# Kernel tuning notes

Measured on AMD Instinct MI355X. Metric: run time of the kernel, lower is better.

Reference implementation:

```python
import jax, jax.numpy as jnp
import numpy as np

K = 32   # tokens_per_obs (hard-coded in module)
V = 512  # vocab_size

def setup_inputs() -> dict:
    key = jax.random.key(0)
    ks = jax.random.split(key, 10)
    s = 0.02  # small init scale for numerical sanity
    return {
        "x": jax.random.normal(ks[0], (4096, 512), jnp.float32),
        "enc_w1": jax.random.normal(ks[1], (512, 512), jnp.float32) * s,
        "enc_b1": jnp.zeros((512,), jnp.float32),
        "enc_w2": jax.random.normal(ks[2], (512, 16384), jnp.float32) * s,
        "enc_b2": jnp.zeros((16384,), jnp.float32),
        "codebook": jax.random.uniform(ks[3], (16384, 256), jnp.float32, -1.0 / V, 1.0 / V),
        "dec_w1": jax.random.normal(ks[4], (256, 512), jnp.float32) * s,
        "dec_b1": jnp.zeros((512,), jnp.float32),
        "dec_w2": jax.random.normal(ks[5], (512, 512), jnp.float32) * s,
        "dec_b2": jnp.zeros((512,), jnp.float32),
    }

def reference(x, enc_w1, enc_b1, enc_w2, enc_b2, codebook,
              dec_w1, dec_b1, dec_w2, dec_b2):
    b = x.shape[0]
    # encoder MLP -> logits z of shape (b, K*V)
    h = jax.nn.relu(x @ enc_w1 + enc_b1)
    z = h @ enc_w2 + enc_b2
    zl = z.reshape(b, K, V)                      # (b, K, V) per-block logits
    # categorical sample per token block
    tokens = jax.random.categorical(jax.random.key(1), zl, axis=-1)  # (b, K) int
    p = jax.nn.softmax(zl, axis=-1).reshape(b, K * V)
    oh = jax.nn.one_hot(tokens, V, dtype=p.dtype).reshape(b, K * V)
    # straight-through: forward value == one-hot, gradient flows through p
    st = p + jax.lax.stop_gradient(oh - p)
    z_q = st @ codebook                          # (b, embed_dim) = sum of K code rows
    # decoder MLP -> reconstruction
    rec = jax.nn.relu(z_q @ dec_w1 + dec_b1) @ dec_w2 + dec_b2
    return z, z_q, rec
```

## Files before the change

### kernel.cpp

```cpp
#include <hip/hip_runtime.h>
#include <hip/hip_bf16.h>
#include <math.h>
#include <stdint.h>


#define BATCH 4096
#define KTOK  32
#define VOCAB 512
#define DMODEL 512
#define ZDIM  16384
#define EDIM  256
#define MARGIN 0.03125f

typedef __attribute__((ext_vector_type(8))) short short8v;
typedef __attribute__((ext_vector_type(4))) float f32x4;

__device__ __forceinline__ void threefry2x32(uint32_t k0, uint32_t k1,
                                             uint32_t x0, uint32_t x1,
                                             uint32_t& y0, uint32_t& y1) {
    uint32_t ks0 = k0, ks1 = k1, ks2 = k0 ^ k1 ^ 0x1BD11BDAu;
    x0 += ks0; x1 += ks1;
#define TFR(r) { x0 += x1; x1 = __builtin_rotateleft32(x1, r); x1 ^= x0; }
    TFR(13) TFR(15) TFR(26) TFR(6)
    x0 += ks1; x1 += ks2 + 1u;
    TFR(17) TFR(29) TFR(16) TFR(24)
    x0 += ks2; x1 += ks0 + 2u;
    TFR(13) TFR(15) TFR(26) TFR(6)
    x0 += ks0; x1 += ks1 + 3u;
    TFR(17) TFR(29) TFR(16) TFR(24)
    x0 += ks1; x1 += ks2 + 4u;
    TFR(13) TFR(15) TFR(26) TFR(6)
    x0 += ks2; x1 += ks0 + 5u;
#undef TFR
    y0 = x0; y1 = x1;
}

__device__ __forceinline__ void threefry4x(uint32_t e,
                                           uint32_t& o0, uint32_t& o1,
                                           uint32_t& o2, uint32_t& o3) {
    const uint32_t KS2 = 0x1BD11BDBu;
    uint32_t xa = 0u, ya = e + 1u;
    uint32_t xb = 0u, yb = e + 2u;
    uint32_t xc = 0u, yc = e + 3u;
    uint32_t xd = 0u, yd = e + 4u;
#define RR(r) \
    xa += ya; xb += yb; xc += yc; xd += yd; \
    ya = __builtin_rotateleft32(ya, r) ^ xa; \
    yb = __builtin_rotateleft32(yb, r) ^ xb; \
    yc = __builtin_rotateleft32(yc, r) ^ xc; \
    yd = __builtin_rotateleft32(yd, r) ^ xd;
    RR(13) RR(15) RR(26) RR(6)
    xa += 1u; xb += 1u; xc += 1u; xd += 1u;
    ya += KS2 + 1u; yb += KS2 + 1u; yc += KS2 + 1u; yd += KS2 + 1u;
    RR(17) RR(29) RR(16) RR(24)
    xa += KS2; xb += KS2; xc += KS2; xd += KS2;
    ya += 2u; yb += 2u; yc += 2u; yd += 2u;
    RR(13) RR(15) RR(26) RR(6)
    ya += 4u; yb += 4u; yc += 4u; yd += 4u;
    RR(17) RR(29) RR(16) RR(24)
    xa += 1u; xb += 1u; xc += 1u; xd += 1u;
    ya += KS2 + 4u; yb += KS2 + 4u; yc += KS2 + 4u; yd += KS2 + 4u;
    RR(13) RR(15) RR(26) RR(6)
    xa += KS2; xb += KS2; xc += KS2; xd += KS2;
    ya += 5u; yb += 5u; yc += 5u; yd += 5u;
#undef RR
    o0 = xa ^ ya; o1 = xb ^ yb; o2 = xc ^ yc; o3 = xd ^ yd;
}

__device__ __forceinline__ float jax_gumbel(uint64_t e) {
    const float TINY = 1.17549435e-38f;
    uint32_t y0, y1;
    threefry2x32(0u, 1u, (uint32_t)(e >> 32), (uint32_t)(e & 0xffffffffull), y0, y1);
    uint32_t bits = y0 ^ y1;
    float u = __uint_as_float(0x3f800000u | (bits >> 9)) - 1.0f;
    u = u * 1.0f + TINY;
    u = fmaxf(TINY, u);
    return -logf(-logf(u));
}

__device__ __forceinline__ float gumbel_from_bits(uint32_t bits) {
    const float TINY = 1.17549435e-38f;
    const float LN2 = 0.69314718056f;
    float f = __uint_as_float(0x3f800000u | (bits >> 9));
    float u = f - 1.0f;
    float d = 2.0f - f;
    u = fmaxf(u, TINY);
    float e_hw = -LN2 * __builtin_amdgcn_logf(u);
    float e_poly = d * fmaf(d, fmaf(d, 0.33333333f, 0.5f), 1.0f);
    float e = (d < 0.002f) ? e_poly : e_hw;
    return -LN2 * __builtin_amdgcn_logf(e);
}

__device__ __forceinline__ float fast_gumbel(uint32_t e32) {
    uint32_t y0, y1;
    threefry2x32(0u, 1u, 0u, e32, y0, y1);
    return gumbel_from_bits(y0 ^ y1);
}

__device__ __forceinline__ unsigned short f32_to_bf16_rne(float f) {
    uint32_t u = __float_as_uint(f);
    uint32_t r = (u + 0x7fffu + ((u >> 16) & 1u)) >> 16;
    return (unsigned short)r;
}

__device__ __forceinline__ void top2_push(float& s1, float& s2, int& v1,
                                          float s, int v) {
    if (s > s1 || (s == s1 && v < v1)) { s2 = s1; s1 = s; v1 = v; }
    else s2 = fmaxf(s2, s);
}
__device__ __forceinline__ void top2_merge(float& s1, float& s2, int& v1,
                                           float os1, float os2, int ov1) {
    if (os1 > s1 || (os1 == s1 && ov1 < v1)) {
        s2 = fmaxf(s1, os2);
        s1 = os1; v1 = ov1;
    } else {
        s2 = fmaxf(s2, os1);
    }
}

__device__ __forceinline__ void gload16(const unsigned short* src,
                                        unsigned short* lds_base) {
    __builtin_amdgcn_global_load_lds(
        (const __attribute__((address_space(1))) unsigned int*)src,
        (__attribute__((address_space(3))) unsigned int*)lds_base, 16, 0, 0);
}

template<bool RELU>
__global__ __launch_bounds__(256)
void gemm_f32_64(const float* __restrict__ A, const float* __restrict__ B,
                 const float* __restrict__ bias, float* __restrict__ C,
                 unsigned short* __restrict__ Cb,
                 int M, int N, int K) {
    constexpr int BK = 16;
    __shared__ __align__(16) float As[BK][68];
    __shared__ __align__(16) float Bs[BK][68];

    const int tid = threadIdx.x;
    const int tx = tid % 16;
    const int ty = tid / 16;
    const int brow = blockIdx.y * 64;
    const int bcol = blockIdx.x * 64;

    float acc[4][4] = {};

    for (int k0 = 0; k0 < K; k0 += BK) {
        {
            int r = tid >> 2, c4 = tid & 3;
            float4 v = *(const float4*)&A[(size_t)(brow + r) * K + k0 + c4 * 4];
            As[c4 * 4 + 0][r] = v.x;
            As[c4 * 4 + 1][r] = v.y;
            As[c4 * 4 + 2][r] = v.z;
            As[c4 * 4 + 3][r] = v.w;
        }
        {
            int r = tid >> 4, c4 = tid & 15;
            *(float4*)&Bs[r][c4 * 4] = *(const float4*)&B[(size_t)(k0 + r) * N + bcol + c4 * 4];
        }
        __syncthreads();

#pragma unroll
        for (int kk = 0; kk < BK; ++kk) {
            float a[4], b[4];
            *(float4*)&a[0] = *(const float4*)&As[kk][ty * 4];
            *(float4*)&b[0] = *(const float4*)&Bs[kk][tx * 4];
#pragma unroll
            for (int i = 0; i < 4; ++i)
#pragma unroll
                for (int j = 0; j < 4; ++j)
                    acc[i][j] = fmaf(a[i], b[j], acc[i][j]);
        }
        __syncthreads();
    }

#pragma unroll
    for (int i = 0; i < 4; ++i) {
        int row = brow + ty * 4 + i;
        int col = bcol + tx * 4;
        float4 v;
        v.x = acc[i][0] + bias[col + 0];
        v.y = acc[i][1] + bias[col + 1];
        v.z = acc[i][2] + bias[col + 2];
        v.w = acc[i][3] + bias[col + 3];
        if (RELU) {
            v.x = fmaxf(v.x, 0.0f); v.y = fmaxf(v.y, 0.0f);
            v.z = fmaxf(v.z, 0.0f); v.w = fmaxf(v.w, 0.0f);
        }
        *(float4*)&C[(size_t)row * N + col] = v;
        if (Cb) {
            ushort4 o;
            o.x = f32_to_bf16_rne(v.x);
            o.y = f32_to_bf16_rne(v.y);
            o.z = f32_to_bf16_rne(v.z);
            o.w = f32_to_bf16_rne(v.w);
            *(ushort4*)&Cb[(size_t)row * N + col] = o;
        }
    }
}

template<bool RELU>
__global__ __launch_bounds__(256)
void gemm_f32(const float* __restrict__ A, const float* __restrict__ B,
              const float* __restrict__ bias, float* __restrict__ C,
              int M, int N, int K) {
    constexpr int BM = 128, BN = 128, BK = 16, TM = 8, TN = 8;
    __shared__ __align__(16) float As[BK][BM + 4];
    __shared__ __align__(16) float Bs[BK][BN + 4];

    const int tid = threadIdx.x;
    const int tx = tid % (BN / TN);
    const int ty = tid / (BN / TN);
    const int brow = blockIdx.y * BM;
    const int bcol = blockIdx.x * BN;

    float acc[TM][TN] = {};

    for (int k0 = 0; k0 < K; k0 += BK) {
#pragma unroll
        for (int f = tid; f < BM * BK / 4; f += 256) {
            int r = f / (BK / 4);
            int c4 = f % (BK / 4);
            float4 v = *(const float4*)&A[(size_t)(brow + r) * K + k0 + c4 * 4];
            As[c4 * 4 + 0][r] = v.x;
            As[c4 * 4 + 1][r] = v.y;
            As[c4 * 4 + 2][r] = v.z;
            As[c4 * 4 + 3][r] = v.w;
        }
#pragma unroll
        for (int f = tid; f < BK * BN / 4; f += 256) {
            int r = f / (BN / 4);
            int c4 = f % (BN / 4);
            *(float4*)&Bs[r][c4 * 4] = *(const float4*)&B[(size_t)(k0 + r) * N + bcol + c4 * 4];
        }
        __syncthreads();

#pragma unroll
        for (int kk = 0; kk < BK; ++kk) {
            float a[TM], b[TN];
            *(float4*)&a[0] = *(const float4*)&As[kk][ty * TM];
            *(float4*)&a[4] = *(const float4*)&As[kk][ty * TM + 4];
            *(float4*)&b[0] = *(const float4*)&Bs[kk][tx * TN];
            *(float4*)&b[4] = *(const float4*)&Bs[kk][tx * TN + 4];
#pragma unroll
            for (int i = 0; i < TM; ++i)
#pragma unroll
                for (int j = 0; j < TN; ++j)
                    acc[i][j] = fmaf(a[i], b[j], acc[i][j]);
        }
        __syncthreads();
    }

#pragma unroll
    for (int i = 0; i < TM; ++i) {
        int row = brow + ty * TM + i;
#pragma unroll
        for (int j = 0; j < TN; j += 4) {
            int col = bcol + tx * TN + j;
            float4 v;
            v.x = acc[i][j + 0] + bias[col + 0];
            v.y = acc[i][j + 1] + bias[col + 1];
            v.z = acc[i][j + 2] + bias[col + 2];
            v.w = acc[i][j + 3] + bias[col + 3];
            if (RELU) {
                v.x = fmaxf(v.x, 0.0f); v.y = fmaxf(v.y, 0.0f);
                v.z = fmaxf(v.z, 0.0f); v.w = fmaxf(v.w, 0.0f);
            }
            *(float4*)&C[(size_t)row * N + col] = v;
        }
    }
}

__global__ __launch_bounds__(256)
void transpose_w2(const float* __restrict__ src, unsigned short* __restrict__ dstb,
                  float* __restrict__ dstf, int R, int C, int writeF) {
    __shared__ float tile[32][33];
    const int c0 = blockIdx.x * 32, r0 = blockIdx.y * 32;
    const int tx = threadIdx.x % 32, ty = threadIdx.x / 32;
#pragma unroll
    for (int i = ty; i < 32; i += 8)
        tile[i][tx] = src[(size_t)(r0 + i) * C + c0 + tx];
    __syncthreads();
#pragma unroll
    for (int i = ty; i < 32; i += 8) {
        float v = tile[tx][i];
        size_t o = (size_t)(c0 + i) * R + r0 + tx;
        dstb[o] = f32_to_bf16_rne(v);
        if (writeF) dstf[o] = v;
    }
}

__global__ __launch_bounds__(256)
void gemm_mfma_bf16(const unsigned short* __restrict__ A,
                    const unsigned short* __restrict__ Bt,
                    const float* __restrict__ bias,
                    float* __restrict__ C,
                    int M, int N, int K) {
    constexpr int BM = 128, BN = 128, BK = 32;
    constexpr int TSZ = BM * BK;
    __shared__ unsigned short As[2 * TSZ];
    __shared__ unsigned short Bs[2 * TSZ];

    const int lid = blockIdx.y * gridDim.x + blockIdx.x;
    const int xcd = lid & 7;
    const int kk2 = lid >> 3;
    const int rpx = gridDim.y >> 3;
    const int by = xcd * rpx + (kk2 % rpx);
    const int bx = kk2 / rpx;

    const int tid = threadIdx.x;
    const int wid = tid >> 6;
    const int lane = tid & 63;
    const int wr = wid >> 1, wc = wid & 1;
    const int l15 = lane & 15, lq = lane >> 4;
    const int brow = by * BM;
    const int bcol = bx * BN;

    const int g1 = tid;
    const int g2 = tid + 256;
    const size_t a1 = (size_t)(brow + (g1 >> 2)) * K + (g1 & 3) * 8;
    const size_t a2 = (size_t)(brow + (g2 >> 2)) * K + (g2 & 3) * 8;
    const size_t b1 = (size_t)(bcol + (g1 >> 2)) * K + (g1 & 3) * 8;
    const size_t b2 = (size_t)(bcol + (g2 >> 2)) * K + (g2 & 3) * 8;
    const int asOff1 = wid * 64 * 8;
    const int asOff2 = (256 + wid * 64) * 8;

    f32x4 acc[4][4];
#pragma unroll
    for (int m = 0; m < 4; ++m)
#pragma unroll
        for (int n = 0; n < 4; ++n) acc[m][n] = (f32x4){0.f, 0.f, 0.f, 0.f};

    const int NK = K / BK;
    gload16(A + a1, As + asOff1);
    gload16(A + a2, As + asOff2);
    gload16(Bt + b1, Bs + asOff1);
    gload16(Bt + b2, Bs + asOff2);
    __syncthreads();

    int buf = 0;
    for (int kt = 0; kt < NK; ++kt) {
        if (kt + 1 < NK) {
            const int k0 = (kt + 1) * BK;
            const int o = (buf ^ 1) * TSZ;
            gload16(A + a1 + k0, As + o + asOff1);
            gload16(A + a2 + k0, As + o + asOff2);
            gload16(Bt + b1 + k0, Bs + o + asOff1);
            gload16(Bt + b2 + k0, Bs + o + asOff2);
        }
        const int cb = buf * TSZ;
        short8v af[4], bf[4];
#pragma unroll
        for (int m = 0; m < 4; ++m)
            af[m] = *(const short8v*)&As[cb + (wr * 64 + m * 16 + l15) * BK + lq * 8];
#pragma unroll
        for (int n = 0; n < 4; ++n)
            bf[n] = *(const short8v*)&Bs[cb + (wc * 64 + n * 16 + l15) * BK + lq * 8];
#pragma unroll
        for (int m = 0; m < 4; ++m)
#pragma unroll
            for (int n = 0; n < 4; ++n)
                acc[m][n] = __builtin_amdgcn_mfma_f32_16x16x32_bf16(
                    af[m], bf[n], acc[m][n], 0, 0, 0);
        __syncthreads();
        buf ^= 1;
    }

#pragma unroll
    for (int m = 0; m < 4; ++m) {
#pragma unroll
        for (int n = 0; n < 4; ++n) {
            int col = bcol + wc * 64 + n * 16 + l15;
            float bv = bias[col];
#pragma unroll
            for (int r = 0; r < 4; ++r) {
                int row = brow + wr * 64 + m * 16 + lq * 4 + r;
                C[(size_t)row * N + col] = acc[m][n][r] + bv;
            }
        }
    }
}

__global__ __launch_bounds__(256)
void sample_tokens_ilp(const float* __restrict__ z, int* __restrict__ tokens,
                       float* __restrict__ s1v, int* __restrict__ amb,
                       int* __restrict__ ambCount) {
    const int wave = threadIdx.x >> 6;
    const int lane = threadIdx.x & 63;
    const uint32_t t = blockIdx.x * 4 + wave;
    const float* zr = z + (size_t)t * VOCAB;

    float s1 = -INFINITY, s2 = -INFINITY;
    int v1 = VOCAB;
#pragma unroll
    for (int half = 0; half < 2; ++half) {
        const int e0 = half * 256 + lane * 4;
        const float4 zv = *(const float4*)&zr[e0];
        uint32_t b0, b1, b2, b3;
        threefry4x(t * (uint32_t)VOCAB + (uint32_t)e0, b0, b1, b2, b3);
        const float g0 = gumbel_from_bits(b0);
        const float g1 = gumbel_from_bits(b1);
        const float g2 = gumbel_from_bits(b2);
        const float g3 = gumbel_from_bits(b3);
        top2_push(s1, s2, v1, zv.x + g0, e0 + 0);
        top2_push(s1, s2, v1, zv.y + g1, e0 + 1);
        top2_push(s1, s2, v1, zv.z + g2, e0 + 2);
        top2_push(s1, s2, v1, zv.w + g3, e0 + 3);
    }
#pragma unroll
    for (int off = 32; off > 0; off >>= 1) {
        float os1 = __shfl_xor(s1, off);
        int ov1 = __shfl_xor(v1, off);
        float os2 = __shfl_xor(s2, off);
        top2_merge(s1, s2, v1, os1, os2, ov1);
    }
    if (lane == 0) {
        tokens[t] = v1;
        s1v[t] = s1;
        if (s1 - s2 < MARGIN) {
            int idx = atomicAdd(ambCount, 1);
            amb[idx] = (int)t;
        }
    }
}

__global__ __launch_bounds__(64)
void refine_tokens2(const float* __restrict__ z, const float* __restrict__ h,
                    const float* __restrict__ w2t, const float* __restrict__ eb2,
                    const int* __restrict__ amb, const int* __restrict__ ambCount,
                    const float* __restrict__ s1v, int* __restrict__ tok) {
    __shared__ float hrow[DMODEL];
    __shared__ int candv[64];
    const int cnt = *ambCount;
    const int lane = threadIdx.x;

    for (int i = blockIdx.x; i < cnt; i += gridDim.x) {
        const int t = amb[i];
        const int b = t >> 5;
        const int kb = t & 31;
        const float* zr = z + (size_t)t * VOCAB;
        const float s1 = s1v[t];

        {
            float4 hv0 = *(const float4*)&h[(size_t)b * DMODEL + lane * 8];
            float4 hv1 = *(const float4*)&h[(size_t)b * DMODEL + lane * 8 + 4];
            *(float4*)&hrow[lane * 8] = hv0;
            *(float4*)&hrow[lane * 8 + 4] = hv1;
        }

        int base = 0;
#pragma unroll
        for (int half = 0; half < 2; ++half) {
            int e0 = half * 256 + lane * 4;
            float4 zv = *(const float4*)&zr[e0];
            float zs[4] = {zv.x, zv.y, zv.z, zv.w};
#pragma unroll
            for (int j = 0; j < 4; ++j) {
                int v = e0 + j;
                float s = zs[j] + fast_gumbel((uint32_t)t * VOCAB + v);
                bool pred = (s >= s1 - MARGIN);
                unsigned long long mask = __ballot(pred);
                if (pred) {
                    int slot = base + __popcll(mask & ((1ull << lane) - 1ull));
                    if (slot < 64) candv[slot] = v;
                }
                base += __popcll(mask);
            }
        }
        __syncthreads();
        const int ncand = base < 64 ? base : 64;

        float bestE = -INFINITY;
        int bestV = VOCAB;
        if (lane < ncand) {
            const int v = candv[lane];
            const int n = kb * VOCAB + v;
            const float* wr_ = w2t + (size_t)n * DMODEL;
            float acc = 0.f;
#pragma unroll 8
            for (int k = 0; k < DMODEL; ++k)
                acc = fmaf(hrow[k], wr_[k], acc);
            bestE = acc + eb2[n] + jax_gumbel((uint64_t)t * VOCAB + v);
            bestV = v;
        }
#pragma unroll
        for (int off = 32; off > 0; off >>= 1) {
            float oe = __shfl_down(bestE, off);
            int ov = __shfl_down(bestV, off);
            if (oe > bestE || (oe == bestE && ov < bestV)) { bestE = oe; bestV = ov; }
        }
        if (lane == 0) tok[t] = bestV;
        __syncthreads();
    }
}

__global__ __launch_bounds__(256)
void sample_tokens_simple(const float* __restrict__ z, int* __restrict__ tokens) {
    const int wave = threadIdx.x >> 6;
    const int lane = threadIdx.x & 63;
    const size_t t = (size_t)blockIdx.x * 4 + wave;
    const float* zr = z + t * VOCAB;
    float zv[8];
    *(float4*)&zv[0] = *(const float4*)&zr[lane * 8];
    *(float4*)&zv[4] = *(const float4*)&zr[lane * 8 + 4];
    const uint64_t ebase = t * (uint64_t)VOCAB + (uint64_t)lane * 8;
    float best = -INFINITY;
    int bestv = 0;
#pragma unroll
    for (int j = 0; j < 8; ++j) {
        float g = jax_gumbel(ebase + j);
        float s = zv[j] + g;
        int v = lane * 8 + j;
        if (s > best || (s == best && v < bestv)) { best = s; bestv = v; }
    }
#pragma unroll
    for (int off = 32; off > 0; off >>= 1) {
        float ob = __shfl_down(best, off);
        int ov = __shfl_down(bestv, off);
        if (ob > best || (ob == best && ov < bestv)) { best = ob; bestv = ov; }
    }
    if (lane == 0) tokens[t] = bestv;
}

__global__ __launch_bounds__(64)
void zero_count(int* p) { if (threadIdx.x == 0) *p = 0; }

__global__ __launch_bounds__(256)
void gather_zq(const int* __restrict__ tokens, const float* __restrict__ codebook,
               float* __restrict__ zq) {
    const int b = blockIdx.x;
    const int d = threadIdx.x;
    float s = 0.0f;
#pragma unroll
    for (int k = 0; k < KTOK; ++k) {
        int tok = tokens[b * KTOK + k];
        s += codebook[(size_t)(k * VOCAB + tok) * EDIM + d];
    }
    zq[(size_t)b * EDIM + d] = s;
}

extern "C" void kernel_launch(void* const* d_in, const int* in_sizes, int n_in,
                              void* d_out, int out_size, void* d_ws, size_t ws_size,
                              hipStream_t stream) {
    const float* x   = (const float*)d_in[0];
    const float* ew1 = (const float*)d_in[1];
    const float* eb1 = (const float*)d_in[2];
    const float* ew2 = (const float*)d_in[3];
    const float* eb2 = (const float*)d_in[4];
    const float* cb  = (const float*)d_in[5];
    const float* dw1 = (const float*)d_in[6];
    const float* db1 = (const float*)d_in[7];
    const float* dw2 = (const float*)d_in[8];
    const float* db2 = (const float*)d_in[9];

    float* out = (float*)d_out;
    float* z   = out;
    float* zq  = out + (size_t)BATCH * ZDIM;
    float* rec = zq + (size_t)BATCH * EDIM;

    char* ws = (char*)d_ws;
    float* h    = (float*)(ws);
    float* h2   = (float*)(ws + 8388608);
    unsigned short* hb   = (unsigned short*)(ws + 16777216);
    unsigned short* w2bt = (unsigned short*)(ws + 20971520);
    float* w2t  = (float*)(ws + 37748736);
    char* tail = ws + 71303168;
    const size_t WS_NEED2 = 71303168 + 1572864 + 256;
    const bool fast2 = ws_size >= WS_NEED2;
    if (!fast2) tail = ws + 16777216;
    int*   tok  = (int*)(tail);
    float* s1v  = (float*)(tail + 524288);
    int*   amb  = (int*)(tail + 1048576);
    int*   cnt  = (int*)(tail + 1572864);

    dim3 blk(256);

    gemm_f32_64<true ><<<dim3(DMODEL / 64, BATCH / 64), blk, 0, stream>>>(
        x, ew1, eb1, h, fast2 ? hb : (unsigned short*)nullptr,
        BATCH, DMODEL, DMODEL);

    if (fast2) {
        transpose_w2<<<dim3(ZDIM / 32, DMODEL / 32), blk, 0, stream>>>(
            ew2, w2bt, w2t, DMODEL, ZDIM, 1);
        zero_count<<<dim3(1), dim3(64), 0, stream>>>(cnt);
        gemm_mfma_bf16<<<dim3(ZDIM / 128, BATCH / 128), blk, 0, stream>>>(
            hb, w2bt, eb2, z, BATCH, ZDIM, DMODEL);
        sample_tokens_ilp<<<dim3(BATCH * KTOK / 4), blk, 0, stream>>>(
            z, tok, s1v, amb, cnt);
        refine_tokens2<<<dim3(4096), dim3(64), 0, stream>>>(
            z, h, w2t, eb2, amb, cnt, s1v, tok);
    } else {
        gemm_f32<false><<<dim3(ZDIM / 128, BATCH / 128), blk, 0, stream>>>(
            h, ew2, eb2, z, BATCH, ZDIM, DMODEL);
        sample_tokens_simple<<<dim3(BATCH * KTOK / 4), blk, 0, stream>>>(z, tok);
    }

    gather_zq<<<dim3(BATCH), blk, 0, stream>>>(tok, cb, zq);

    gemm_f32_64<true ><<<dim3(DMODEL / 64, BATCH / 64), blk, 0, stream>>>(
        zq, dw1, db1, h2, nullptr, BATCH, DMODEL, EDIM);
    gemm_f32_64<false><<<dim3(DMODEL / 64, BATCH / 64), blk, 0, stream>>>(
        h2, dw2, db2, rec, nullptr, BATCH, DMODEL, DMODEL);
}
```

Baseline: 435.1 us.

## Triple-buffer MFMA GEMM, use bf16 MFMA for decoder, simplify sampling top-1

```diff
diff --git a/kernel.cpp b/kernel.cpp
--- a/kernel.cpp
+++ b/kernel.cpp
@@ -103,21 +103,6 @@
     return (unsigned short)r;
 }
 
-__device__ __forceinline__ void top2_push(float& s1, float& s2, int& v1,
-                                          float s, int v) {
-    if (s > s1 || (s == s1 && v < v1)) { s2 = s1; s1 = s; v1 = v; }
-    else s2 = fmaxf(s2, s);
-}
-__device__ __forceinline__ void top2_merge(float& s1, float& s2, int& v1,
-                                           float os1, float os2, int ov1) {
-    if (os1 > s1 || (os1 == s1 && ov1 < v1)) {
-        s2 = fmaxf(s1, os2);
-        s1 = os1; v1 = ov1;
-    } else {
-        s2 = fmaxf(s2, os1);
-    }
-}
-
 __device__ __forceinline__ void gload16(const unsigned short* src,
                                         unsigned short* lds_base) {
     __builtin_amdgcn_global_load_lds(
@@ -288,16 +273,17 @@
     }
 }
 
+template<bool RELU, bool WF32, bool WBF16>
 __global__ __launch_bounds__(256)
-void gemm_mfma_bf16(const unsigned short* __restrict__ A,
-                    const unsigned short* __restrict__ Bt,
-                    const float* __restrict__ bias,
-                    float* __restrict__ C,
-                    int M, int N, int K) {
+void gemm_mfma(const unsigned short* __restrict__ A,
+               const unsigned short* __restrict__ Bt,
+               const float* __restrict__ bias,
+               float* __restrict__ C, unsigned short* __restrict__ Cb,
+               int M, int N, int K) {
     constexpr int BM = 128, BN = 128, BK = 32;
     constexpr int TSZ = BM * BK;
-    __shared__ unsigned short As[2 * TSZ];
-    __shared__ unsigned short Bs[2 * TSZ];
+    __shared__ unsigned short As[3 * TSZ];
+    __shared__ unsigned short Bs[3 * TSZ];
 
     const int lid = blockIdx.y * gridDim.x + blockIdx.x;
     const int xcd = lid & 7;
@@ -320,8 +306,8 @@
     const size_t a2 = (size_t)(brow + (g2 >> 2)) * K + (g2 & 3) * 8;
     const size_t b1 = (size_t)(bcol + (g1 >> 2)) * K + (g1 & 3) * 8;
     const size_t b2 = (size_t)(bcol + (g2 >> 2)) * K + (g2 & 3) * 8;
-    const int asOff1 = wid * 64 * 8;
-    const int asOff2 = (256 + wid * 64) * 8;
+    const int off1 = wid * 64 * 8;
+    const int off2 = (256 + wid * 64) * 8;
 
     f32x4 acc[4][4];
 #pragma unroll
@@ -330,22 +316,30 @@
         for (int n = 0; n < 4; ++n) acc[m][n] = (f32x4){0.f, 0.f, 0.f, 0.f};
 
     const int NK = K / BK;
-    gload16(A + a1, As + asOff1);
-    gload16(A + a2, As + asOff2);
-    gload16(Bt + b1, Bs + asOff1);
-    gload16(Bt + b2, Bs + asOff2);
-    __syncthreads();
+
+#define STAGE(kt, bufi) { \
+    const int k0_ = (kt) * BK; \
+    const int o_ = (bufi) * TSZ; \
+    gload16(A + a1 + k0_, As + o_ + off1); \
+    gload16(A + a2 + k0_, As + o_ + off2); \
+    gload16(Bt + b1 + k0_, Bs + o_ + off1); \
+    gload16(Bt + b2 + k0_, Bs + o_ + off2); }
+
+    STAGE(0, 0)
+    if (NK > 1) STAGE(1, 1)
 
     int buf = 0;
     for (int kt = 0; kt < NK; ++kt) {
-        if (kt + 1 < NK) {
-            const int k0 = (kt + 1) * BK;
-            const int o = (buf ^ 1) * TSZ;
-            gload16(A + a1 + k0, As + o + asOff1);
-            gload16(A + a2 + k0, As + o + asOff2);
-            gload16(Bt + b1 + k0, Bs + o + asOff1);
-            gload16(Bt + b2 + k0, Bs + o + asOff2);
-        }
+        if (kt + 2 < NK) {
+            int nb = buf + 2; if (nb >= 3) nb -= 3;
+            STAGE(kt + 2, nb)
+        }
+        if (kt + 2 < NK)      asm volatile("s_waitcnt vmcnt(8)" ::: "memory");
+        else if (kt + 1 < NK) asm volatile("s_waitcnt vmcnt(4)" ::: "memory");
+        else                  asm volatile("s_waitcnt vmcnt(0)" ::: "memory");
+        __builtin_amdgcn_s_barrier();
+        __builtin_amdgcn_sched_barrier(0);
+
         const int cb = buf * TSZ;
         short8v af[4], bf[4];
 #pragma unroll
@@ -360,9 +354,10 @@
             for (int n = 0; n < 4; ++n)
                 acc[m][n] = __builtin_amdgcn_mfma_f32_16x16x32_bf16(
                     af[m], bf[n], acc[m][n], 0, 0, 0);
-        __syncthreads();
-        buf ^= 1;
-    }
+        __builtin_amdgcn_s_barrier();
+        ++buf; if (buf == 3) buf = 0;
+    }
+#undef STAGE
 
 #pragma unroll
     for (int m = 0; m < 4; ++m) {
@@ -373,14 +368,17 @@
 #pragma unroll
             for (int r = 0; r < 4; ++r) {
                 int row = brow + wr * 64 + m * 16 + lq * 4 + r;
-                C[(size_t)row * N + col] = acc[m][n][r] + bv;
+                float v = acc[m][n][r] + bv;
+                if (RELU) v = fmaxf(v, 0.0f);
+                if (WF32) C[(size_t)row * N + col] = v;
+                if (WBF16) Cb[(size_t)row * N + col] = f32_to_bf16_rne(v);
             }
         }
     }
 }
 
 __global__ __launch_bounds__(256)
-void sample_tokens_ilp(const float* __restrict__ z, int* __restrict__ tokens,
+void sample_tokens_max(const float* __restrict__ z, int* __restrict__ tokens,
                        float* __restrict__ s1v, int* __restrict__ amb,
                        int* __restrict__ ambCount) {
     const int wave = threadIdx.x >> 6;
@@ -388,34 +386,42 @@
     const uint32_t t = blockIdx.x * 4 + wave;
     const float* zr = z + (size_t)t * VOCAB;
 
-    float s1 = -INFINITY, s2 = -INFINITY;
-    int v1 = VOCAB;
+    float sc[8];
+    float m = -INFINITY;
 #pragma unroll
     for (int half = 0; half < 2; ++half) {
         const int e0 = half * 256 + lane * 4;
         const float4 zv = *(const float4*)&zr[e0];
         uint32_t b0, b1, b2, b3;
         threefry4x(t * (uint32_t)VOCAB + (uint32_t)e0, b0, b1, b2, b3);
-        const float g0 = gumbel_from_bits(b0);
-        const float g1 = gumbel_from_bits(b1);
-        const float g2 = gumbel_from_bits(b2);
-        const float g3 = gumbel_from_bits(b3);
-        top2_push(s1, s2, v1, zv.x + g0, e0 + 0);
-        top2_push(s1, s2, v1, zv.y + g1, e0 + 1);
-        top2_push(s1, s2, v1, zv.z + g2, e0 + 2);
-        top2_push(s1, s2, v1, zv.w + g3, e0 + 3);
-    }
-#pragma unroll
-    for (int off = 32; off > 0; off >>= 1) {
-        float os1 = __shfl_xor(s1, off);
-        int ov1 = __shfl_xor(v1, off);
-        float os2 = __shfl_xor(s2, off);
-        top2_merge(s1, s2, v1, os1, os2, ov1);
+        sc[half * 4 + 0] = zv.x + gumbel_from_bits(b0);
+        sc[half * 4 + 1] = zv.y + gumbel_from_bits(b1);
+        sc[half * 4 + 2] = zv.z + gumbel_from_bits(b2);
+        sc[half * 4 + 3] = zv.w + gumbel_from_bits(b3);
+        m = fmaxf(m, fmaxf(fmaxf(sc[half * 4 + 0], sc[half * 4 + 1]),
+                           fmaxf(sc[half * 4 + 2], sc[half * 4 + 3])));
+    }
+#pragma unroll
+    for (int off = 32; off > 0; off >>= 1)
+        m = fmaxf(m, __shfl_xor(m, off));
+
+    const float thr = m - MARGIN;
+    int nge = 0;
+    int vsel = VOCAB;
+#pragma unroll
+    for (int idx = 0; idx < 8; ++idx) {
+        unsigned long long mge = __ballot(sc[idx] >= thr);
+        nge += __popcll(mge);
+        unsigned long long meq = __ballot(sc[idx] == m);
+        if (vsel == VOCAB && meq) {
+            int ln = __builtin_ctzll(meq);
+            vsel = (idx >> 2) * 256 + ln * 4 + (idx & 3);
+        }
     }
     if (lane == 0) {
-        tokens[t] = v1;
-        s1v[t] = s1;
-        if (s1 - s2 < MARGIN) {
+        tokens[t] = vsel;
+        s1v[t] = m;
+        if (nge >= 2) {
             int idx = atomicAdd(ambCount, 1);
             amb[idx] = (int)t;
         }
@@ -525,7 +531,7 @@
 
 __global__ __launch_bounds__(256)
 void gather_zq(const int* __restrict__ tokens, const float* __restrict__ codebook,
-               float* __restrict__ zq) {
+               float* __restrict__ zq, unsigned short* __restrict__ zqb) {
     const int b = blockIdx.x;
     const int d = threadIdx.x;
     float s = 0.0f;
@@ -535,6 +541,7 @@
         s += codebook[(size_t)(k * VOCAB + tok) * EDIM + d];
     }
     zq[(size_t)b * EDIM + d] = s;
+    if (zqb) zqb[(size_t)b * EDIM + d] = f32_to_bf16_rne(s);
 }
 
 extern "C" void kernel_launch(void* const* d_in, const int* in_sizes, int n_in,
@@ -558,7 +565,11 @@
 
     char* ws = (char*)d_ws;
     float* h    = (float*)(ws);
-    float* h2   = (float*)(ws + 8388608);
+    unsigned short* zqb   = (unsigned short*)(ws + 8388608);
+    unsigned short* h2b   = (unsigned short*)(ws + 10485760);
+    unsigned short* dw1tb = (unsigned short*)(ws + 14680064);
+    unsigned short* dw2tb = (unsigned short*)(ws + 14942208);
+    float* h2f  = (float*)(ws + 8388608);
     unsigned short* hb   = (unsigned short*)(ws + 16777216);
     unsigned short* w2bt = (unsigned short*)(ws + 20971520);
     float* w2t  = (float*)(ws + 37748736);
@@ -580,23 +591,30 @@
     if (fast2) {
         transpose_w2<<<dim3(ZDIM / 32, DMODEL / 32), blk, 0, stream>>>(
             ew2, w2bt, w2t, DMODEL, ZDIM, 1);
+        transpose_w2<<<dim3(DMODEL / 32, EDIM / 32), blk, 0, stream>>>(
+            dw1, dw1tb, nullptr, EDIM, DMODEL, 0);
+        transpose_w2<<<dim3(DMODEL / 32, DMODEL / 32), blk, 0, stream>>>(
+            dw2, dw2tb, nullptr, DMODEL, DMODEL, 0);
         zero_count<<<dim3(1), dim3(64), 0, stream>>>(cnt);
-        gemm_mfma_bf16<<<dim3(ZDIM / 128, BATCH / 128), blk, 0, stream>>>(
-            hb, w2bt, eb2, z, BATCH, ZDIM, DMODEL);
-        sample_tokens_ilp<<<dim3(BATCH * KTOK / 4), blk, 0, stream>>>(
+        gemm_mfma<false, true, false><<<dim3(ZDIM / 128, BATCH / 128), blk, 0, stream>>>(
+            hb, w2bt, eb2, z, nullptr, BATCH, ZDIM, DMODEL);
+        sample_tokens_max<<<dim3(BATCH * KTOK / 4), blk, 0, stream>>>(
             z, tok, s1v, amb, cnt);
         refine_tokens2<<<dim3(4096), dim3(64), 0, stream>>>(
             z, h, w2t, eb2, amb, cnt, s1v, tok);
+        gather_zq<<<dim3(BATCH), blk, 0, stream>>>(tok, cb, zq, zqb);
+        gemm_mfma<true, false, true><<<dim3(DMODEL / 128, BATCH / 128), blk, 0, stream>>>(
+            zqb, dw1tb, db1, nullptr, h2b, BATCH, DMODEL, EDIM);
+        gemm_mfma<false, true, false><<<dim3(DMODEL / 128, BATCH / 128), blk, 0, stream>>>(
+            h2b, dw2tb, db2, rec, nullptr, BATCH, DMODEL, DMODEL);
     } else {
         gemm_f32<false><<<dim3(ZDIM / 128, BATCH / 128), blk, 0, stream>>>(
             h, ew2, eb2, z, BATCH, ZDIM, DMODEL);
         sample_tokens_simple<<<dim3(BATCH * KTOK / 4), blk, 0, stream>>>(z, tok);
-    }
-
-    gather_zq<<<dim3(BATCH), blk, 0, stream>>>(tok, cb, zq);
-
-    gemm_f32_64<true ><<<dim3(DMODEL / 64, BATCH / 64), blk, 0, stream>>>(
-        zq, dw1, db1, h2, nullptr, BATCH, DMODEL, EDIM);
-    gemm_f32_64<false><<<dim3(DMODEL / 64, BATCH / 64), blk, 0, stream>>>(
-        h2, dw2, db2, rec, nullptr, BATCH, DMODEL, DMODEL);
-}
+        gather_zq<<<dim3(BATCH), blk, 0, stream>>>(tok, cb, zq, nullptr);
+        gemm_f32_64<true ><<<dim3(DMODEL / 64, BATCH / 64), blk, 0, stream>>>(
+            zq, dw1, db1, h2f, nullptr, BATCH, DMODEL, EDIM);
+        gemm_f32_64<false><<<dim3(DMODEL / 64, BATCH / 64), blk, 0, stream>>>(
+            h2f, dw2, db2, rec, nullptr, BATCH, DMODEL, DMODEL);
+    }
+}
```

Result: faster. 395.2 us (median of 2 runs) (-9.2%).
